# Kernel optimization log

Measured on AMD Instinct MI355X. Metric: run time of the kernel, lower is better.

The kernel has to match this reference:

```python
import jax, jax.numpy as jnp
import numpy as np
import math

SR = 16000
FFT = 1024
WIN = 640
HOP = 320
NMEL = 40
NCEP = 13
B = 1024
NS = 16000
F_MIN = 0.0
F_MAX = 8000.0
LIFT_L = 22.0
DELTA_N = 2


def _linear_to_mel_weight_matrix(num_mel, num_spec_bins, sr, fmin, fmax):
    # Exact replica of tf.signal.linear_to_mel_weight_matrix (HTK mel scale).
    def hz_to_mel(f):
        return 1127.0 * np.log1p(np.asarray(f, np.float64) / 700.0)
    nyquist = sr / 2.0
    lin_freqs = np.linspace(0.0, nyquist, num_spec_bins)
    spec_mel = hz_to_mel(lin_freqs[1:])[:, None]          # drop DC bin
    edges = np.linspace(hz_to_mel(fmin), hz_to_mel(fmax), num_mel + 2)
    lower, center, upper = edges[:-2], edges[1:-1], edges[2:]
    lower_slope = (spec_mel - lower) / (center - lower)
    upper_slope = (upper - spec_mel) / (upper - center)
    w = np.maximum(0.0, np.minimum(lower_slope, upper_slope))
    w = np.pad(w, ((1, 0), (0, 0)))                       # re-add zero DC row
    return w.astype(np.float32)


def setup_inputs() -> dict:
    key = jax.random.key(0)
    waveforms = jax.random.normal(key, (B, NS), dtype=jnp.float32)
    mel_fb = jnp.asarray(_linear_to_mel_weight_matrix(NMEL, FFT // 2 + 1, SR, F_MIN, F_MAX))
    return {"waveforms": waveforms, "mel_fb": mel_fb}


def _delta(feat, N):
    # feat: (B, T, C). Replicate-pad N frames at both ends, then weighted
    # sliding-window sum with weights k in [-N..N] (vectorized, no map_fn).
    T = feat.shape[1]
    denom = 2.0 * sum(float(k * k) for k in range(1, N + 1))
    padded = jnp.concatenate(
        [jnp.repeat(feat[:, :1, :], N, axis=1), feat,
         jnp.repeat(feat[:, -1:, :], N, axis=1)], axis=1)
    acc = jnp.zeros_like(feat)
    for k in range(-N, N + 1):
        if k != 0:
            acc = acc + float(k) * padded[:, N + k:N + k + T, :]
    return acc / denom


def reference(waveforms, mel_fb):
    # --- STFT (tf.signal.stft: periodic Hann, no pad_end, zero-pad to FFT) ---
    n = jnp.arange(WIN, dtype=jnp.float32)
    window = 0.5 - 0.5 * jnp.cos(2.0 * math.pi * n / WIN)
    num_frames = 1 + (NS - WIN) // HOP                    # 49
    idx = jnp.arange(num_frames)[:, None] * HOP + jnp.arange(WIN)[None, :]
    frames = waveforms[:, idx] * window
    frames = jnp.pad(frames, ((0, 0), (0, 0), (0, FFT - WIN)))
    spec = jnp.abs(jnp.fft.rfft(frames, n=FFT, axis=-1))  # (B, T, 513)

    # --- mel + log ---
    log_mel = jnp.log(spec @ mel_fb + 1e-6)               # (B, T, NMEL)

    # --- MFCC: DCT-II scaled by rsqrt(2*NMEL), keep first NCEP coeffs ---
    m = jnp.arange(NMEL, dtype=jnp.float32)[:, None]
    k = jnp.arange(NCEP, dtype=jnp.float32)[None, :]
    dct_mat = 2.0 * jnp.cos(math.pi * (2.0 * m + 1.0) * k / (2.0 * NMEL))
    mfccs = (log_mel @ dct_mat) * (1.0 / math.sqrt(2.0 * NMEL))

    # --- liftering ---
    c = jnp.arange(NCEP, dtype=jnp.float32)
    lift = 1.0 + (LIFT_L / 2.0) * jnp.sin(math.pi * c / LIFT_L)
    mfccs = mfccs * lift

    # --- deltas and delta-deltas ---
    d1 = _delta(mfccs, DELTA_N)
    d2 = _delta(d1, DELTA_N)
    out = jnp.concatenate([mfccs, d1, d2], axis=2)        # (B, T, 3*NCEP)
    return out[..., None]                                 # (B, T, 39, 1)
```

## Files before the change

kernel.cpp:

```cpp
#include <hip/hip_runtime.h>
#include <math.h>

#define NMEL   40
#define NCEP   13
#define BATCH  1024
#define NSAMP  16000
#define NFRAME 49
#define PI_F   3.14159265358979323846f

#define WS_WIN  0
#define WS_R    640
#define WS_DT   1664
#define WS_BT   2184
#define WS_TOT  15240

typedef _Float16 half8 __attribute__((ext_vector_type(8)));
typedef __fp16   fp16x2 __attribute__((ext_vector_type(2)));
typedef float f32x4 __attribute__((ext_vector_type(4)));

#define FFT_SB() __builtin_amdgcn_sched_barrier(0x77)

#define BFLY(i0, i1, wr, wi) {                        \
    float tr = zr[i0] - zr[i1], ti = zi[i0] - zi[i1]; \
    zr[i0] += zr[i1]; zi[i0] += zi[i1];               \
    zr[i1] = tr*(wr) - ti*(wi);                       \
    zi[i1] = tr*(wi) + ti*(wr); }

__device__ __forceinline__ unsigned pk_f16(float a, float b) {
    fp16x2 h = __builtin_amdgcn_cvt_pkrtz(a, b);
    union { fp16x2 h; unsigned u; } cvt; cvt.h = h;
    return cvt.u;
}

__global__ __launch_bounds__(256) void mfcc_prep(
    const float* __restrict__ mel_fb, float* __restrict__ ws)
{
    const int idx = blockIdx.x * 256 + threadIdx.x;

    _Float16* bt = (_Float16*)(ws + WS_BT);
    for (int i = idx; i < 48 * 544; i += 64 * 256) {
        int n = i / 544, k = i - n * 544;
        float v = (n < NMEL && k < 513) ? mel_fb[k * NMEL + n] : 0.0f;
        bt[i] = (_Float16)v;
    }

    if (idx < 640 + 512 + 520) {
        int i = idx;
        if (i < 640) {
            ws[WS_WIN + i] = 0.5f - 0.5f * cosf(2.0f * PI_F * (float)i / 640.0f);
        } else if (i < 1152) {
            int k = i - 640;
            float s, c;
            sincosf(-2.0f * PI_F * (float)k / 1024.0f, &s, &c);
            ((float2*)(ws + WS_R))[k] = make_float2(c, s);
        } else {
            int j = i - 1152;
            int m = j / 13, c0 = j - m * 13;
            float d    = 2.0f * cosf(PI_F * (2.0f * m + 1.0f) * (float)c0 / 80.0f);
            float lift = 1.0f + 11.0f * sinf(PI_F * (float)c0 / 22.0f);
            ws[WS_DT + j] = d * 0.11180339887498949f * lift;
        }
    }
}

__global__ __launch_bounds__(256) void mfcc_stage1(
    const float* __restrict__ wave, const float* __restrict__ ws,
    float* __restrict__ out)
{
    __shared__ __align__(16) char smem[4 * 640 * 8 + 16 * 40 * 2];
    char* smemc = smem;
    _Float16* lm = (_Float16*)(smem + 4 * 640 * 8);

    const int tid = threadIdx.x;
    const int wv  = tid >> 6;
    const int L   = tid & 63;
    const int s   = L & 7;
    const int a   = L >> 3;

    float2* Z = (float2*)smem + wv * 640;
    const float2* R   = (const float2*)(ws + WS_R);
    const float2* win = (const float2*)(ws + WS_WIN);

    float2 twA[4], twB[2], twC, twD[4], twE[2], twF, twS[8], winv[5];
    #pragma unroll
    for (int j = 0; j < 4; ++j) twA[j] = R[2 * (L + 64 * j)];
    #pragma unroll
    for (int j = 0; j < 2; ++j) twB[j] = R[4 * (L + 64 * j)];
    twC = R[8 * L];
    #pragma unroll
    for (int j = 0; j < 4; ++j) twD[j] = R[128 * j + 16 * s];
    #pragma unroll
    for (int j = 0; j < 2; ++j) twE[j] = R[256 * j + 32 * s];
    twF = R[64 * s];
    #pragma unroll
    for (int j = 0; j < 8; ++j) twS[j] = R[8 * L + j];
    #pragma unroll
    for (int j = 0; j < 5; ++j) winv[j] = win[L + 64 * j];

    uint4 mgp[4];
    float m512v[4] = {0.0f, 0.0f, 0.0f, 0.0f};

    float2 xv[5];
    {
        const int frame = blockIdx.x * 16 + wv * 4;
        const int b = frame / NFRAME;
        const int f = frame - b * NFRAME;
        const float2* xp = (const float2*)(wave + (size_t)b * NSAMP + (size_t)f * 320);
        #pragma unroll
        for (int j = 0; j < 5; ++j) xv[j] = xp[L + 64 * j];
    }

    #pragma unroll
    for (int fi = 0; fi < 4; ++fi) {
        float2 xn[5];
        if (fi < 3) {
            const int frame = blockIdx.x * 16 + wv * 4 + fi + 1;
            const int b = frame / NFRAME;
            const int f = frame - b * NFRAME;
            const float2* xp = (const float2*)(wave + (size_t)b * NSAMP + (size_t)f * 320);
            #pragma unroll
            for (int j = 0; j < 5; ++j) xn[j] = xp[L + 64 * j];
        }

        float zr[8], zi[8];
        #pragma unroll
        for (int j = 0; j < 8; ++j) { zr[j] = 0.0f; zi[j] = 0.0f; }
        #pragma unroll
        for (int j = 0; j < 5; ++j) {
            zr[j] = xv[j].x * winv[j].x;
            zi[j] = xv[j].y * winv[j].y;
        }

        #pragma unroll
        for (int j = 0; j < 4; ++j) BFLY(j, j + 4, twA[j].x, twA[j].y);
        #pragma unroll
        for (int g = 0; g < 8; g += 4) {
            #pragma unroll
            for (int j = 0; j < 2; ++j) BFLY(g + j, g + j + 2, twB[j].x, twB[j].y);
        }
        #pragma unroll
        for (int i0 = 0; i0 < 8; i0 += 2) BFLY(i0, i0 + 1, twC.x, twC.y);

        FFT_SB();
        #pragma unroll
        for (int j = 0; j < 8; ++j)
            Z[80 * j + 10 * s + a] = make_float2(zr[j], zi[j]);
        FFT_SB();
        {
            float4 q0 = *(float4*)&Z[10 * L + 0];
            float4 q1 = *(float4*)&Z[10 * L + 2];
            float4 q2 = *(float4*)&Z[10 * L + 4];
            float4 q3 = *(float4*)&Z[10 * L + 6];
            zr[0] = q0.x; zi[0] = q0.y; zr[1] = q0.z; zi[1] = q0.w;
            zr[2] = q1.x; zi[2] = q1.y; zr[3] = q1.z; zi[3] = q1.w;
            zr[4] = q2.x; zi[4] = q2.y; zr[5] = q2.z; zi[5] = q2.w;
            zr[6] = q3.x; zi[6] = q3.y; zr[7] = q3.z; zi[7] = q3.w;
        }

        #pragma unroll
        for (int j = 0; j < 4; ++j) BFLY(j, j + 4, twD[j].x, twD[j].y);
        #pragma unroll
        for (int g = 0; g < 8; g += 4) {
            #pragma unroll
            for (int j = 0; j < 2; ++j) BFLY(g + j, g + j + 2, twE[j].x, twE[j].y);
        }
        #pragma unroll
        for (int i0 = 0; i0 < 8; i0 += 2) BFLY(i0, i0 + 1, twF.x, twF.y);

        FFT_SB();
        #pragma unroll
        for (int j = 0; j < 8; ++j)
            Z[80 * a + 10 * j + s] = make_float2(zr[j], zi[j]);
        FFT_SB();
        {
            float4 q0 = *(float4*)&Z[10 * L + 0];
            float4 q1 = *(float4*)&Z[10 * L + 2];
            float4 q2 = *(float4*)&Z[10 * L + 4];
            float4 q3 = *(float4*)&Z[10 * L + 6];
            zr[0] = q0.x; zi[0] = q0.y; zr[1] = q0.z; zi[1] = q0.w;
            zr[2] = q1.x; zi[2] = q1.y; zr[3] = q1.z; zi[3] = q1.w;
            zr[4] = q2.x; zi[4] = q2.y; zr[5] = q2.z; zi[5] = q2.w;
            zr[6] = q3.x; zi[6] = q3.y; zr[7] = q3.z; zi[7] = q3.w;
        }

        {
            const float C = 0.70710678118654752f;
            const float w8r[4] = { 1.0f,  C, 0.0f, -C };
            const float w8i[4] = { 0.0f, -C, -1.0f, -C };
            #pragma unroll
            for (int j = 0; j < 4; ++j) BFLY(j, j + 4, w8r[j], w8i[j]);
            #pragma unroll
            for (int g = 0; g < 8; g += 4) {
                BFLY(g + 0, g + 2, 1.0f, 0.0f);
                BFLY(g + 1, g + 3, 0.0f, -1.0f);
            }
            #pragma unroll
            for (int i0 = 0; i0 < 8; i0 += 2) BFLY(i0, i0 + 1, 1.0f, 0.0f);
        }

        FFT_SB();
        {
            const int rev3t[8] = { 0, 4, 2, 6, 1, 5, 3, 7 };
            int r6 = (int)(__brev((unsigned)L) >> 26);
            int u  = r6 + 2 * (r6 >> 3);
            #pragma unroll
            for (int j = 0; j < 8; ++j)
                Z[80 * rev3t[j] + u] = make_float2(zr[j], zi[j]);
        }
        FFT_SB();

        float Ax[8], Ay[8], Bx[8], By[8];
        {
            float4 a0 = *(float4*)&Z[10 * L + 0];
            float4 a1 = *(float4*)&Z[10 * L + 2];
            float4 a2 = *(float4*)&Z[10 * L + 4];
            float4 a3 = *(float4*)&Z[10 * L + 6];
            Ax[0] = a0.x; Ay[0] = a0.y; Ax[1] = a0.z; Ay[1] = a0.w;
            Ax[2] = a1.x; Ay[2] = a1.y; Ax[3] = a1.z; Ay[3] = a1.w;
            Ax[4] = a2.x; Ay[4] = a2.y; Ax[5] = a2.z; Ay[5] = a2.w;
            Ax[6] = a3.x; Ay[6] = a3.y; Ax[7] = a3.z; Ay[7] = a3.w;
            float4 t0 = *(float4*)&Z[630 - 10 * L + 0];
            float4 t1 = *(float4*)&Z[630 - 10 * L + 2];
            float4 t2 = *(float4*)&Z[630 - 10 * L + 4];
            float4 t3 = *(float4*)&Z[630 - 10 * L + 6];
            float2 b0 = Z[640 - 10 * L];
            Bx[0] = b0.x;  By[0] = b0.y;
            Bx[7] = t0.z;  By[7] = t0.w;
            Bx[6] = t1.x;  By[6] = t1.y;
            Bx[5] = t1.z;  By[5] = t1.w;
            Bx[4] = t2.x;  By[4] = t2.y;
            Bx[3] = t2.z;  By[3] = t2.w;
            Bx[2] = t3.x;  By[2] = t3.y;
            Bx[1] = t3.z;  By[1] = t3.w;
        }
        float mg[8];
        #pragma unroll
        for (int j = 0; j < 8; ++j) {
            int k = 8 * L + j;
            if (k == 0) {
                mg[j]     = fabsf(Ax[0] + Ay[0]);
                m512v[fi] = fabsf(Ax[0] - Ay[0]);
            } else {
                float xer = 0.5f * (Ax[j] + Bx[j]), xei = 0.5f * (Ay[j] - By[j]);
                float xo  = 0.5f * (Ay[j] + By[j]), xoi = -0.5f * (Ax[j] - Bx[j]);
                float xr = xer + twS[j].x * xo - twS[j].y * xoi;
                float xi = xei + twS[j].x * xoi + twS[j].y * xo;
                mg[j] = sqrtf(xr * xr + xi * xi);
            }
        }
        mgp[fi].x = pk_f16(mg[0], mg[1]);
        mgp[fi].y = pk_f16(mg[2], mg[3]);
        mgp[fi].z = pk_f16(mg[4], mg[5]);
        mgp[fi].w = pk_f16(mg[6], mg[7]);
        FFT_SB();

        if (fi < 3) {
            #pragma unroll
            for (int j = 0; j < 5; ++j) xv[j] = xn[j];
        }
    }

    __syncthreads();
    #pragma unroll
    for (int fi = 0; fi < 4; ++fi) {
        const int row = wv * 4 + fi;
        *(uint4*)(smemc + row * 1104 + 16 * L) = mgp[fi];
        if (L < 20) {
            unsigned v = (L == 0) ? pk_f16(m512v[fi], 0.0f) : 0u;
            *(unsigned*)(smemc + row * 1104 + 1024 + 4 * L) = v;
        }
    }
    __syncthreads();

    if (wv < 3) {
        const int nl = L & 15, q = L >> 4;
        const char* ap = smemc + nl * 1104 + q * 16;
        const _Float16* btp = (const _Float16*)(ws + WS_BT)
                              + (size_t)(wv * 16 + nl) * 544 + q * 8;
        f32x4 acc = {0.0f, 0.0f, 0.0f, 0.0f};
        #pragma unroll
        for (int kk = 0; kk < 17; ++kk) {
            half8 av = *(const half8*)(ap + kk * 64);
            half8 bv = *(const half8*)(btp + kk * 32);
            acc = __builtin_amdgcn_mfma_f32_16x16x32_f16(av, bv, acc, 0, 0, 0);
        }
        const int mel = wv * 16 + nl;
        if (mel < NMEL) {
            #pragma unroll
            for (int r = 0; r < 4; ++r) {
                int fl = q * 4 + r;
                lm[fl * NMEL + mel] = (_Float16)__logf(acc[r] + 1e-6f);
            }
        }
    }
    __syncthreads();

    if (tid < 16 * NCEP) {
        const int fl = tid / NCEP, c = tid - fl * NCEP;
        float acc = 0.0f;
        #pragma unroll
        for (int m = 0; m < NMEL; ++m)
            acc += (float)lm[fl * NMEL + m] * ws[WS_DT + m * 13 + c];
        out[(size_t)(blockIdx.x * 16 + fl) * (3 * NCEP) + c] = acc;
    }
}

__global__ __launch_bounds__(128) void mfcc_stage2(float* __restrict__ out)
{
    __shared__ float x [NFRAME * NCEP];
    __shared__ float d1[NFRAME * NCEP];

    const int b = blockIdx.x;
    const int tid = threadIdx.x;
    const int TC = NFRAME * NCEP;

    for (int i = tid; i < TC; i += 128) {
        const int t = i / NCEP, c = i - t * NCEP;
        x[i] = out[((size_t)b * NFRAME + t) * (3 * NCEP) + c];
    }
    __syncthreads();

    for (int i = tid; i < TC; i += 128) {
        const int t = i / NCEP, c = i - t * NCEP;
        float acc = 0.0f;
        #pragma unroll
        for (int k = -2; k <= 2; ++k) {
            if (k == 0) continue;
            int tt = t + k;
            tt = tt < 0 ? 0 : (tt > NFRAME - 1 ? NFRAME - 1 : tt);
            acc += (float)k * x[tt * NCEP + c];
        }
        d1[i] = acc * 0.1f;
    }
    __syncthreads();

    for (int i = tid; i < TC; i += 128) {
        const int t = i / NCEP, c = i - t * NCEP;
        float acc = 0.0f;
        #pragma unroll
        for (int k = -2; k <= 2; ++k) {
            if (k == 0) continue;
            int tt = t + k;
            tt = tt < 0 ? 0 : (tt > NFRAME - 1 ? NFRAME - 1 : tt);
            acc += (float)k * d1[tt * NCEP + c];
        }
        const size_t base = ((size_t)b * NFRAME + t) * (3 * NCEP);
        out[base +     NCEP + c] = d1[i];
        out[base + 2 * NCEP + c] = acc * 0.1f;
    }
}

extern "C" void kernel_launch(void* const* d_in, const int* in_sizes, int n_in,
                              void* d_out, int out_size, void* d_ws, size_t ws_size,
                              hipStream_t stream)
{
    const float* wave   = (const float*)d_in[0];
    const float* mel_fb = (const float*)d_in[1];
    float* out = (float*)d_out;
    float* ws  = (float*)d_ws;

    mfcc_prep<<<64, 256, 0, stream>>>(mel_fb, ws);
    mfcc_stage1<<<(BATCH * NFRAME) / 16, 256, 0, stream>>>(wave, ws, out);
    mfcc_stage2<<<BATCH, 128, 0, stream>>>(out);
}
```

Measured before the change: 168.4 us.

## Interleave two frames per FFT pass and place log-mel scratch after magnitudes

Restructures the per-wave FFT loop so each iteration processes two frames in lockstep, alternating their butterfly phases and LDS transposes. The aim is to hide LDS write/read latency and expose more independent arithmetic. Prefetching now loads two frames ahead, and the log-mel scratch is moved to reuse the FFT buffer region past the magnitude rows, shrinking shared memory. In exchange, register pressure rises from holding two frames' state plus prefetched samples, which could cause spills or lower occupancy. Both frames share the same Z scratch sequentially, which relies on in-wave ordering.

```diff
diff --git a/kernel.cpp b/kernel.cpp
--- a/kernel.cpp
+++ b/kernel.cpp
@@ -63,13 +63,163 @@
     }
 }
 
+__device__ __forceinline__ void ldFrame(float2 (&x)[5], const float* __restrict__ wave,
+                                        int frame, int L)
+{
+    const int b = frame / NFRAME;
+    const int f = frame - b * NFRAME;
+    const float2* xp = (const float2*)(wave + (size_t)b * NSAMP + (size_t)f * 320);
+    #pragma unroll
+    for (int j = 0; j < 5; ++j) x[j] = xp[L + 64 * j];
+}
+
+__device__ __forceinline__ void phaseI(float (&zr)[8], float (&zi)[8],
+    const float2 (&xv)[5], const float2 (&winv)[5],
+    const float2 (&twA)[4], const float2 (&twB)[2], const float2 twC)
+{
+    #pragma unroll
+    for (int j = 0; j < 8; ++j) { zr[j] = 0.0f; zi[j] = 0.0f; }
+    #pragma unroll
+    for (int j = 0; j < 5; ++j) { zr[j] = xv[j].x * winv[j].x; zi[j] = xv[j].y * winv[j].y; }
+    #pragma unroll
+    for (int j = 0; j < 4; ++j) BFLY(j, j + 4, twA[j].x, twA[j].y);
+    #pragma unroll
+    for (int g = 0; g < 8; g += 4) {
+        #pragma unroll
+        for (int j = 0; j < 2; ++j) BFLY(g + j, g + j + 2, twB[j].x, twB[j].y);
+    }
+    #pragma unroll
+    for (int i0 = 0; i0 < 8; i0 += 2) BFLY(i0, i0 + 1, twC.x, twC.y);
+}
+
+__device__ __forceinline__ void phaseII(float (&zr)[8], float (&zi)[8],
+    const float4 (&q)[4],
+    const float2 (&twD)[4], const float2 (&twE)[2], const float2 twF)
+{
+    zr[0] = q[0].x; zi[0] = q[0].y; zr[1] = q[0].z; zi[1] = q[0].w;
+    zr[2] = q[1].x; zi[2] = q[1].y; zr[3] = q[1].z; zi[3] = q[1].w;
+    zr[4] = q[2].x; zi[4] = q[2].y; zr[5] = q[2].z; zi[5] = q[2].w;
+    zr[6] = q[3].x; zi[6] = q[3].y; zr[7] = q[3].z; zi[7] = q[3].w;
+    #pragma unroll
+    for (int j = 0; j < 4; ++j) BFLY(j, j + 4, twD[j].x, twD[j].y);
+    #pragma unroll
+    for (int g = 0; g < 8; g += 4) {
+        #pragma unroll
+        for (int j = 0; j < 2; ++j) BFLY(g + j, g + j + 2, twE[j].x, twE[j].y);
+    }
+    #pragma unroll
+    for (int i0 = 0; i0 < 8; i0 += 2) BFLY(i0, i0 + 1, twF.x, twF.y);
+}
+
+__device__ __forceinline__ void phaseIII(float (&zr)[8], float (&zi)[8],
+    const float4 (&q)[4])
+{
+    zr[0] = q[0].x; zi[0] = q[0].y; zr[1] = q[0].z; zi[1] = q[0].w;
+    zr[2] = q[1].x; zi[2] = q[1].y; zr[3] = q[1].z; zi[3] = q[1].w;
+    zr[4] = q[2].x; zi[4] = q[2].y; zr[5] = q[2].z; zi[5] = q[2].w;
+    zr[6] = q[3].x; zi[6] = q[3].y; zr[7] = q[3].z; zi[7] = q[3].w;
+    const float C = 0.70710678118654752f;
+    const float w8r[4] = { 1.0f,  C, 0.0f, -C };
+    const float w8i[4] = { 0.0f, -C, -1.0f, -C };
+    #pragma unroll
+    for (int j = 0; j < 4; ++j) BFLY(j, j + 4, w8r[j], w8i[j]);
+    #pragma unroll
+    for (int g = 0; g < 8; g += 4) {
+        BFLY(g + 0, g + 2, 1.0f, 0.0f);
+        BFLY(g + 1, g + 3, 0.0f, -1.0f);
+    }
+    #pragma unroll
+    for (int i0 = 0; i0 < 8; i0 += 2) BFLY(i0, i0 + 1, 1.0f, 0.0f);
+}
+
+__device__ __forceinline__ void wrEx1(float2* Z, const float (&zr)[8], const float (&zi)[8],
+                                      int s, int a)
+{
+    #pragma unroll
+    for (int j = 0; j < 8; ++j) Z[80 * j + 10 * s + a] = make_float2(zr[j], zi[j]);
+}
+
+__device__ __forceinline__ void wrEx2(float2* Z, const float (&zr)[8], const float (&zi)[8],
+                                      int s, int a)
+{
+    #pragma unroll
+    for (int j = 0; j < 8; ++j) Z[80 * a + 10 * j + s] = make_float2(zr[j], zi[j]);
+}
+
+__device__ __forceinline__ void wrEx3(float2* Z, const float (&zr)[8], const float (&zi)[8],
+                                      int u)
+{
+    const int rev3t[8] = { 0, 4, 2, 6, 1, 5, 3, 7 };
+    #pragma unroll
+    for (int j = 0; j < 8; ++j) Z[80 * rev3t[j] + u] = make_float2(zr[j], zi[j]);
+}
+
+__device__ __forceinline__ void rdEx(const float2* Z, int L, float4 (&q)[4])
+{
+    q[0] = *(const float4*)&Z[10 * L + 0];
+    q[1] = *(const float4*)&Z[10 * L + 2];
+    q[2] = *(const float4*)&Z[10 * L + 4];
+    q[3] = *(const float4*)&Z[10 * L + 6];
+}
+
+__device__ __forceinline__ void rdMag(const float2* Z, int L,
+    float4 (&aq)[4], float4 (&tq)[4], float2& b0)
+{
+    aq[0] = *(const float4*)&Z[10 * L + 0];
+    aq[1] = *(const float4*)&Z[10 * L + 2];
+    aq[2] = *(const float4*)&Z[10 * L + 4];
+    aq[3] = *(const float4*)&Z[10 * L + 6];
+    tq[0] = *(const float4*)&Z[630 - 10 * L + 0];
+    tq[1] = *(const float4*)&Z[630 - 10 * L + 2];
+    tq[2] = *(const float4*)&Z[630 - 10 * L + 4];
+    tq[3] = *(const float4*)&Z[630 - 10 * L + 6];
+    b0    = Z[640 - 10 * L];
+}
+
+__device__ __forceinline__ void magPhase(const float4 (&aq)[4], const float4 (&tq)[4],
+    const float2 b0, const float2 (&twS)[8], const int L, uint4& mgpo, float& m512o)
+{
+    float Ax[8], Ay[8], Bx[8], By[8];
+    Ax[0] = aq[0].x; Ay[0] = aq[0].y; Ax[1] = aq[0].z; Ay[1] = aq[0].w;
+    Ax[2] = aq[1].x; Ay[2] = aq[1].y; Ax[3] = aq[1].z; Ay[3] = aq[1].w;
+    Ax[4] = aq[2].x; Ay[4] = aq[2].y; Ax[5] = aq[2].z; Ay[5] = aq[2].w;
+    Ax[6] = aq[3].x; Ay[6] = aq[3].y; Ax[7] = aq[3].z; Ay[7] = aq[3].w;
+    Bx[0] = b0.x;    By[0] = b0.y;
+    Bx[7] = tq[0].z; By[7] = tq[0].w;
+    Bx[6] = tq[1].x; By[6] = tq[1].y;
+    Bx[5] = tq[1].z; By[5] = tq[1].w;
+    Bx[4] = tq[2].x; By[4] = tq[2].y;
+    Bx[3] = tq[2].z; By[3] = tq[2].w;
+    Bx[2] = tq[3].x; By[2] = tq[3].y;
+    Bx[1] = tq[3].z; By[1] = tq[3].w;
+    float mg[8];
+    #pragma unroll
+    for (int j = 0; j < 8; ++j) {
+        int k = 8 * L + j;
+        if (k == 0) {
+            mg[j]  = fabsf(Ax[0] + Ay[0]);
+            m512o  = fabsf(Ax[0] - Ay[0]);
+        } else {
+            float xer = 0.5f * (Ax[j] + Bx[j]), xei = 0.5f * (Ay[j] - By[j]);
+            float xo  = 0.5f * (Ay[j] + By[j]), xoi = -0.5f * (Ax[j] - Bx[j]);
+            float xr = xer + twS[j].x * xo - twS[j].y * xoi;
+            float xi = xei + twS[j].x * xoi + twS[j].y * xo;
+            mg[j] = sqrtf(xr * xr + xi * xi);
+        }
+    }
+    mgpo.x = pk_f16(mg[0], mg[1]);
+    mgpo.y = pk_f16(mg[2], mg[3]);
+    mgpo.z = pk_f16(mg[4], mg[5]);
+    mgpo.w = pk_f16(mg[6], mg[7]);
+}
+
 __global__ __launch_bounds__(256) void mfcc_stage1(
     const float* __restrict__ wave, const float* __restrict__ ws,
     float* __restrict__ out)
 {
-    __shared__ __align__(16) char smem[4 * 640 * 8 + 16 * 40 * 2];
+    __shared__ __align__(16) char smem[4 * 640 * 8 + 16];
     char* smemc = smem;
-    _Float16* lm = (_Float16*)(smem + 4 * 640 * 8);
+    _Float16* lm = (_Float16*)(smem + 16 * 1104);
 
     const int tid = threadIdx.x;
     const int wv  = tid >> 6;
@@ -97,166 +247,72 @@
     #pragma unroll
     for (int j = 0; j < 5; ++j) winv[j] = win[L + 64 * j];
 
+    const int r6 = (int)(__brev((unsigned)L) >> 26);
+    const int u  = r6 + 2 * (r6 >> 3);
+
     uint4 mgp[4];
     float m512v[4] = {0.0f, 0.0f, 0.0f, 0.0f};
 
-    float2 xv[5];
-    {
-        const int frame = blockIdx.x * 16 + wv * 4;
-        const int b = frame / NFRAME;
-        const int f = frame - b * NFRAME;
-        const float2* xp = (const float2*)(wave + (size_t)b * NSAMP + (size_t)f * 320);
-        #pragma unroll
-        for (int j = 0; j < 5; ++j) xv[j] = xp[L + 64 * j];
-    }
-
-    #pragma unroll
-    for (int fi = 0; fi < 4; ++fi) {
-        float2 xn[5];
-        if (fi < 3) {
-            const int frame = blockIdx.x * 16 + wv * 4 + fi + 1;
-            const int b = frame / NFRAME;
-            const int f = frame - b * NFRAME;
-            const float2* xp = (const float2*)(wave + (size_t)b * NSAMP + (size_t)f * 320);
+    const int fbase = blockIdx.x * 16 + wv * 4;
+
+    float2 xA[5], xB[5];
+    ldFrame(xA, wave, fbase + 0, L);
+    ldFrame(xB, wave, fbase + 1, L);
+
+    #pragma unroll
+    for (int p = 0; p < 2; ++p) {
+        float2 xA2[5], xB2[5];
+        if (p == 0) {
+            ldFrame(xA2, wave, fbase + 2, L);
+            ldFrame(xB2, wave, fbase + 3, L);
+        }
+
+        float zrA[8], ziA[8], zrB[8], ziB[8];
+        float4 qA[4], qB[4];
+
+        phaseI(zrA, ziA, xA, winv, twA, twB, twC);
+        FFT_SB();
+        wrEx1(Z, zrA, ziA, s, a);
+        FFT_SB();
+        rdEx(Z, L, qA);
+        FFT_SB();
+        phaseI(zrB, ziB, xB, winv, twA, twB, twC);
+        wrEx1(Z, zrB, ziB, s, a);
+        FFT_SB();
+        rdEx(Z, L, qB);
+        FFT_SB();
+
+        phaseII(zrA, ziA, qA, twD, twE, twF);
+        wrEx2(Z, zrA, ziA, s, a);
+        FFT_SB();
+        rdEx(Z, L, qA);
+        FFT_SB();
+        phaseII(zrB, ziB, qB, twD, twE, twF);
+        wrEx2(Z, zrB, ziB, s, a);
+        FFT_SB();
+        rdEx(Z, L, qB);
+        FFT_SB();
+
+        phaseIII(zrA, ziA, qA);
+        wrEx3(Z, zrA, ziA, u);
+        FFT_SB();
+        float4 aqA[4], tqA[4]; float2 b0A;
+        rdMag(Z, L, aqA, tqA, b0A);
+        FFT_SB();
+        phaseIII(zrB, ziB, qB);
+        wrEx3(Z, zrB, ziB, u);
+        FFT_SB();
+        float4 aqB[4], tqB[4]; float2 b0B;
+        rdMag(Z, L, aqB, tqB, b0B);
+        FFT_SB();
+
+        magPhase(aqA, tqA, b0A, twS, L, mgp[2 * p + 0], m512v[2 * p + 0]);
+        magPhase(aqB, tqB, b0B, twS, L, mgp[2 * p + 1], m512v[2 * p + 1]);
+        FFT_SB();
+
+        if (p == 0) {
             #pragma unroll
-            for (int j = 0; j < 5; ++j) xn[j] = xp[L + 64 * j];
-        }
-
-        float zr[8], zi[8];
-        #pragma unroll
-        for (int j = 0; j < 8; ++j) { zr[j] = 0.0f; zi[j] = 0.0f; }
-        #pragma unroll
-        for (int j = 0; j < 5; ++j) {
-            zr[j] = xv[j].x * winv[j].x;
-            zi[j] = xv[j].y * winv[j].y;
-        }
-
-        #pragma unroll
-        for (int j = 0; j < 4; ++j) BFLY(j, j + 4, twA[j].x, twA[j].y);
-        #pragma unroll
-        for (int g = 0; g < 8; g += 4) {
-            #pragma unroll
-            for (int j = 0; j < 2; ++j) BFLY(g + j, g + j + 2, twB[j].x, twB[j].y);
-        }
-        #pragma unroll
-        for (int i0 = 0; i0 < 8; i0 += 2) BFLY(i0, i0 + 1, twC.x, twC.y);
-
-        FFT_SB();
-        #pragma unroll
-        for (int j = 0; j < 8; ++j)
-            Z[80 * j + 10 * s + a] = make_float2(zr[j], zi[j]);
-        FFT_SB();
-        {
-            float4 q0 = *(float4*)&Z[10 * L + 0];
-            float4 q1 = *(float4*)&Z[10 * L + 2];
-            float4 q2 = *(float4*)&Z[10 * L + 4];
-            float4 q3 = *(float4*)&Z[10 * L + 6];
-            zr[0] = q0.x; zi[0] = q0.y; zr[1] = q0.z; zi[1] = q0.w;
-            zr[2] = q1.x; zi[2] = q1.y; zr[3] = q1.z; zi[3] = q1.w;
-            zr[4] = q2.x; zi[4] = q2.y; zr[5] = q2.z; zi[5] = q2.w;
-            zr[6] = q3.x; zi[6] = q3.y; zr[7] = q3.z; zi[7] = q3.w;
-        }
-
-        #pragma unroll
-        for (int j = 0; j < 4; ++j) BFLY(j, j + 4, twD[j].x, twD[j].y);
-        #pragma unroll
-        for (int g = 0; g < 8; g += 4) {
-            #pragma unroll
-            for (int j = 0; j < 2; ++j) BFLY(g + j, g + j + 2, twE[j].x, twE[j].y);
-        }
-        #pragma unroll
-        for (int i0 = 0; i0 < 8; i0 += 2) BFLY(i0, i0 + 1, twF.x, twF.y);
-
-        FFT_SB();
-        #pragma unroll
-        for (int j = 0; j < 8; ++j)
-            Z[80 * a + 10 * j + s] = make_float2(zr[j], zi[j]);
-        FFT_SB();
-        {
-            float4 q0 = *(float4*)&Z[10 * L + 0];
-            float4 q1 = *(float4*)&Z[10 * L + 2];
-            float4 q2 = *(float4*)&Z[10 * L + 4];
-            float4 q3 = *(float4*)&Z[10 * L + 6];
-            zr[0] = q0.x; zi[0] = q0.y; zr[1] = q0.z; zi[1] = q0.w;
-            zr[2] = q1.x; zi[2] = q1.y; zr[3] = q1.z; zi[3] = q1.w;
-            zr[4] = q2.x; zi[4] = q2.y; zr[5] = q2.z; zi[5] = q2.w;
-            zr[6] = q3.x; zi[6] = q3.y; zr[7] = q3.z; zi[7] = q3.w;
-        }
-
-        {
-            const float C = 0.70710678118654752f;
-            const float w8r[4] = { 1.0f,  C, 0.0f, -C };
-            const float w8i[4] = { 0.0f, -C, -1.0f, -C };
-            #pragma unroll
-            for (int j = 0; j < 4; ++j) BFLY(j, j + 4, w8r[j], w8i[j]);
-            #pragma unroll
-            for (int g = 0; g < 8; g += 4) {
-                BFLY(g + 0, g + 2, 1.0f, 0.0f);
-                BFLY(g + 1, g + 3, 0.0f, -1.0f);
-            }
-            #pragma unroll
-            for (int i0 = 0; i0 < 8; i0 += 2) BFLY(i0, i0 + 1, 1.0f, 0.0f);
-        }
-
-        FFT_SB();
-        {
-            const int rev3t[8] = { 0, 4, 2, 6, 1, 5, 3, 7 };
-            int r6 = (int)(__brev((unsigned)L) >> 26);
-            int u  = r6 + 2 * (r6 >> 3);
-            #pragma unroll
-            for (int j = 0; j < 8; ++j)
-                Z[80 * rev3t[j] + u] = make_float2(zr[j], zi[j]);
-        }
-        FFT_SB();
-
-        float Ax[8], Ay[8], Bx[8], By[8];
-        {
-            float4 a0 = *(float4*)&Z[10 * L + 0];
-            float4 a1 = *(float4*)&Z[10 * L + 2];
-            float4 a2 = *(float4*)&Z[10 * L + 4];
-            float4 a3 = *(float4*)&Z[10 * L + 6];
-            Ax[0] = a0.x; Ay[0] = a0.y; Ax[1] = a0.z; Ay[1] = a0.w;
-            Ax[2] = a1.x; Ay[2] = a1.y; Ax[3] = a1.z; Ay[3] = a1.w;
-            Ax[4] = a2.x; Ay[4] = a2.y; Ax[5] = a2.z; Ay[5] = a2.w;
-            Ax[6] = a3.x; Ay[6] = a3.y; Ax[7] = a3.z; Ay[7] = a3.w;
-            float4 t0 = *(float4*)&Z[630 - 10 * L + 0];
-            float4 t1 = *(float4*)&Z[630 - 10 * L + 2];
-            float4 t2 = *(float4*)&Z[630 - 10 * L + 4];
-            float4 t3 = *(float4*)&Z[630 - 10 * L + 6];
-            float2 b0 = Z[640 - 10 * L];
-            Bx[0] = b0.x;  By[0] = b0.y;
-            Bx[7] = t0.z;  By[7] = t0.w;
-            Bx[6] = t1.x;  By[6] = t1.y;
-            Bx[5] = t1.z;  By[5] = t1.w;
-            Bx[4] = t2.x;  By[4] = t2.y;
-            Bx[3] = t2.z;  By[3] = t2.w;
-            Bx[2] = t3.x;  By[2] = t3.y;
-            Bx[1] = t3.z;  By[1] = t3.w;
-        }
-        float mg[8];
-        #pragma unroll
-        for (int j = 0; j < 8; ++j) {
-            int k = 8 * L + j;
-            if (k == 0) {
-                mg[j]     = fabsf(Ax[0] + Ay[0]);
-                m512v[fi] = fabsf(Ax[0] - Ay[0]);
-            } else {
-                float xer = 0.5f * (Ax[j] + Bx[j]), xei = 0.5f * (Ay[j] - By[j]);
-                float xo  = 0.5f * (Ay[j] + By[j]), xoi = -0.5f * (Ax[j] - Bx[j]);
-                float xr = xer + twS[j].x * xo - twS[j].y * xoi;
-                float xi = xei + twS[j].x * xoi + twS[j].y * xo;
-                mg[j] = sqrtf(xr * xr + xi * xi);
-            }
-        }
-        mgp[fi].x = pk_f16(mg[0], mg[1]);
-        mgp[fi].y = pk_f16(mg[2], mg[3]);
-        mgp[fi].z = pk_f16(mg[4], mg[5]);
-        mgp[fi].w = pk_f16(mg[6], mg[7]);
-        FFT_SB();
-
-        if (fi < 3) {
-            #pragma unroll
-            for (int j = 0; j < 5; ++j) xv[j] = xn[j];
+            for (int j = 0; j < 5; ++j) { xA[j] = xA2[j]; xB[j] = xB2[j]; }
         }
     }
 
```

Result: faster. 163.2 us (-3.1%).
